# Kernel optimization log

Hardware: AMD Instinct MI355X
Metric: run time of the kernel (lower is better)

Reference implementation:

```python
import jax, jax.numpy as jnp
import numpy as np

# dims chosen per input_specs / init_kwargs
B, S, D_IN, UNITS, WIN = 4, 2048, 512, 64, 32
W = 2 * WIN + 1  # max window length


def setup_inputs() -> dict:
    key = jax.random.key(0)
    ks = jax.random.split(key, 8)
    p = lambda k, shape: jax.random.normal(k, shape, dtype=jnp.float32) * 0.02
    return {
        "query": jax.random.normal(ks[0], (B, S, D_IN), dtype=jnp.float32),
        "value": jax.random.normal(ks[1], (B, S, D_IN), dtype=jnp.float32),
        "Wq": p(ks[2], (D_IN, UNITS)), "bq": jnp.zeros((UNITS,), jnp.float32),
        "Wk": p(ks[3], (D_IN, UNITS)), "bk": jnp.zeros((UNITS,), jnp.float32),
        "Wv": p(ks[4], (D_IN, UNITS)), "bv": jnp.zeros((UNITS,), jnp.float32),
    }


def reference(query, value, Wq, bq, Wk, bk, Wv, bv):
    # Dense projections (query stream -> Q, value stream -> K and V)
    Q = query @ Wq + bq
    K = value @ Wk + bk
    V = value @ Wv + bv

    i = np.arange(S)
    start = np.maximum(i - WIN, 0)            # [S]
    end = np.minimum(i + WIN + 1, S)          # [S]
    lengths = end - start                      # [S] window length per position
    offsets = np.concatenate([[0], np.cumsum(lengths)[:-1]])
    L = int(lengths.sum())                     # total output seq length (concat of all windows)

    idx = start[:, None] + np.arange(W)[None, :]   # [S, W] window token indices
    valid = idx < end[:, None]                      # [S, W] which slots exist
    idx_c = np.minimum(idx, S - 1)                  # clamp for safe gather

    idx_c = jnp.asarray(idx_c)
    valid_j = jnp.asarray(valid)

    # Gather overlapping windows: [B, S, W, UNITS]
    Ql = Q[:, idx_c]
    Kl = K[:, idx_c]
    Vl = V[:, idx_c]

    # Faithful to original: ALL window rows act as queries for window i.
    scale = 1.0 / jnp.sqrt(jnp.asarray(UNITS, dtype=Q.dtype))
    scores = jnp.einsum("bswd,bsud->bswu", Ql, Kl) * scale  # [B, S, W, W]
    neg = jnp.finfo(scores.dtype).min
    scores = jnp.where(valid_j[None, :, None, :], scores, neg)  # mask padded keys
    weights = jax.nn.softmax(scores, axis=-1)
    out_local = jnp.einsum("bswu,bsud->bswd", weights, Vl)  # [B, S, W, UNITS]

    # Concat valid rows of every window along seq axis -> [B, L, UNITS]
    flat_pos = jnp.asarray(offsets)[:, None] + jnp.arange(W)[None, :]  # [S, W]
    flat_pos = jnp.where(valid_j, flat_pos, L)  # invalid rows dumped in slot L
    out = jnp.zeros((Q.shape[0], L + 1, UNITS), dtype=out_local.dtype)
    out = out.at[:, flat_pos.reshape(-1)].set(out_local.reshape(Q.shape[0], -1, UNITS))
    return out[:, :L]
```

## Files before the change

### kernel.cpp

```cpp
#include <hip/hip_runtime.h>
#include <hip/hip_bf16.h>

#define BB 4
#define SS 2048
#define DIN 512
#define UU 64
#define WINR 32
#define LTOT 132064
#define GQ 4
#define NWP 132

typedef __attribute__((ext_vector_type(8))) short short8;
typedef __attribute__((ext_vector_type(4))) float float4v;

static __device__ __forceinline__ ushort f2bf(float f) {
    union { __hip_bfloat16 h; ushort u; } c;
    c.h = __float2bfloat16(f);
    return c.u;
}
static __device__ __forceinline__ float bf2f(ushort u) {
    union { float f; uint v; } c;
    c.v = ((uint)u) << 16;
    return c.f;
}

__device__ __forceinline__ int offs_of(int s) {
    int a = s < (SS - 33) ? s : (SS - 33);
    int m = (s - 33) > 0 ? (s - 33) : 0;
    return a * (a - 1) / 2 + 33 * a + (s - a) * SS - m * (m + 1) / 2;
}

__global__ __launch_bounds__(256) void prep_w(
    const float* __restrict__ Wq, const float* __restrict__ Wk, const float* __restrict__ Wv,
    ushort* __restrict__ Wt)
{
    __shared__ float T[64][65];
    const int mtx = blockIdx.x >> 3;
    const int kc  = blockIdx.x & 7;
    const float* W = (mtx == 0) ? Wq : ((mtx == 1) ? Wk : Wv);
    const int tid = threadIdx.x;
    for (int idx = tid; idx < 64 * 64; idx += 256) {
        const int k = idx >> 6, n = idx & 63;
        T[n][k] = W[(size_t)(kc * 64 + k) * UU + n];
    }
    __syncthreads();
    for (int idx = tid; idx < 64 * 64; idx += 256) {
        const int n = idx >> 6, kl = idx & 63;
        Wt[(size_t)mtx * UU * DIN + (size_t)n * DIN + kc * 64 + kl] = f2bf(T[n][kl]);
    }
}

__global__ __launch_bounds__(64) void qkv_mfma(
    const float* __restrict__ query, const float* __restrict__ value,
    const ushort* __restrict__ Wt,
    const float* __restrict__ bq, const float* __restrict__ bk, const float* __restrict__ bv,
    float* __restrict__ Qs, ushort* __restrict__ Kf, ushort* __restrict__ Vf)
{
    const int bid = blockIdx.x;
    const int mtx = bid >> 9;
    const int rt  = bid & 511;
    const int lane = threadIdx.x;
    const int m16 = lane & 15, quad = lane >> 4;

    const float* X = (mtx == 0) ? query : value;
    const float* Xrow = X + (size_t)(rt * 16 + m16) * DIN + quad * 8;
    const ushort* Wm = Wt + (size_t)mtx * UU * DIN + (size_t)m16 * DIN + quad * 8;

    float4v acc[4];
#pragma unroll
    for (int nb = 0; nb < 4; ++nb) acc[nb] = (float4v){0.f, 0.f, 0.f, 0.f};

#pragma unroll
    for (int kk = 0; kk < 16; ++kk) {
        const float4 xa = *(const float4*)(Xrow + kk * 32);
        const float4 xb = *(const float4*)(Xrow + kk * 32 + 4);
        short8 a;
        a[0] = (short)f2bf(xa.x); a[1] = (short)f2bf(xa.y);
        a[2] = (short)f2bf(xa.z); a[3] = (short)f2bf(xa.w);
        a[4] = (short)f2bf(xb.x); a[5] = (short)f2bf(xb.y);
        a[6] = (short)f2bf(xb.z); a[7] = (short)f2bf(xb.w);
#pragma unroll
        for (int nb = 0; nb < 4; ++nb) {
            const short8 bfr = *(const short8*)(Wm + (size_t)nb * 16 * DIN + kk * 32);
            acc[nb] = __builtin_amdgcn_mfma_f32_16x16x32_bf16(a, bfr, acc[nb], 0, 0, 0);
        }
    }

    const float* bias = (mtx == 0) ? bq : ((mtx == 1) ? bk : bv);
    const int r0 = rt * 16 + quad * 4;
#pragma unroll
    for (int nb = 0; nb < 4; ++nb) {
        const int col = nb * 16 + m16;
        const float bv_ = bias[col];
        if (mtx == 0) {
#pragma unroll
            for (int reg = 0; reg < 4; ++reg)
                Qs[(size_t)(r0 + reg) * UU + col] = (acc[nb][reg] + bv_) * 0.125f;
        } else if (mtx == 1) {
#pragma unroll
            for (int reg = 0; reg < 4; ++reg)
                Kf[(size_t)(r0 + reg) * UU + col] = f2bf(acc[nb][reg] + bv_);
        } else {
#pragma unroll
            for (int reg = 0; reg < 4; ++reg)
                Vf[(size_t)(r0 + reg) * UU + col] = f2bf(acc[nb][reg] + bv_);
        }
    }
}

__global__ __launch_bounds__(512) void attn_kernel(
    const float* __restrict__ Qs, const ushort* __restrict__ Kf,
    const ushort* __restrict__ Vf, float* __restrict__ out)
{
    constexpr int STRIDE = 66;
    __shared__ ushort Kl[NWP * STRIDE];
    __shared__ ushort Vl[NWP * STRIDE];
    __shared__ float ev[GQ][NWP];
    __shared__ float qr[GQ][UU];

    const int blk = blockIdx.x;
    const int b = blk >> 9;
    const int q0 = (blk & 511) << 2;
    const int tid = threadIdx.x;

    const int j0 = max(q0 - 2 * WINR, 0);
    const int j1 = min(q0 + GQ - 1 + 2 * WINR + 1, SS);
    const int nw = j1 - j0;

    if (tid < GQ * UU) {
        const int g = tid >> 6, d = tid & 63;
        qr[g][d] = Qs[((size_t)b * SS + q0 + g) * UU + d];
    }
    const uint* Kg = (const uint*)(Kf + ((size_t)b * SS + j0) * UU);
    const uint* Vg = (const uint*)(Vf + ((size_t)b * SS + j0) * UU);
    for (int idx = tid; idx < nw * 32; idx += 512) {
        const int j = idx >> 5, d2 = idx & 31;
        ((uint*)(Kl + j * STRIDE))[d2] = Kg[idx];
        ((uint*)(Vl + j * STRIDE))[d2] = Vg[idx];
    }
    __syncthreads();

    for (int item = tid; item < GQ * NWP; item += 512) {
        const int g = item / NWP, jj = item - g * NWP;
        float e = 0.f;
        if (jj < nw) {
            const uint* kr = (const uint*)(Kl + jj * STRIDE);
            const float* q = qr[g];
            float dot = 0.f;
#pragma unroll
            for (int p = 0; p < UU / 2; ++p) {
                const uint kp = kr[p];
                dot = fmaf(q[2 * p],     bf2f((ushort)kp),         dot);
                dot = fmaf(q[2 * p + 1], bf2f((ushort)(kp >> 16)), dot);
            }
            e = __expf(dot);
        }
        ev[g][jj] = e;
    }
    __syncthreads();

    const int w = tid >> 6, lane = tid & 63;
    const int g = w >> 1, h = w & 1;
    const int qi = q0 + g;
    const int s_lo = max(qi - WINR, 0);
    const int s_hi = min(qi + WINR, SS - 1);
    const int ns = s_hi - s_lo + 1;
    const int half = (ns + 1) >> 1;
    const int sa = s_lo + h * half;
    const int sb = h ? s_hi : (s_lo + half - 1);

    int st = max(sa - WINR, 0);
    int en = min(sa + WINR + 1, SS);
    float acc = 0.f, den = 0.f;
    const float* evg = ev[g];
    for (int j = st; j < en; ++j) {
        const float e = evg[j - j0];
        acc = fmaf(e, bf2f(Vl[(j - j0) * STRIDE + lane]), acc);
        den += e;
    }
    int off = offs_of(sa);
    float* outb = out + (size_t)b * LTOT * UU;
    for (int s = sa;; ++s) {
        outb[(size_t)(off + (qi - st)) * UU + lane] = acc * __builtin_amdgcn_rcpf(den);
        if (s == sb) break;
        off += en - st;
        if (en < SS) {
            const float e = evg[en - j0];
            acc = fmaf(e, bf2f(Vl[(en - j0) * STRIDE + lane]), acc);
            den += e;
            ++en;
        }
        if (s + 1 > WINR) {
            const float e = evg[st - j0];
            acc = fmaf(-e, bf2f(Vl[(st - j0) * STRIDE + lane]), acc);
            den -= e;
            ++st;
        }
    }
}

extern "C" void kernel_launch(void* const* d_in, const int* in_sizes, int n_in,
                              void* d_out, int out_size, void* d_ws, size_t ws_size,
                              hipStream_t stream) {
    const float* query = (const float*)d_in[0];
    const float* value = (const float*)d_in[1];
    const float* Wq = (const float*)d_in[2];
    const float* bq = (const float*)d_in[3];
    const float* Wk = (const float*)d_in[4];
    const float* bk = (const float*)d_in[5];
    const float* Wv = (const float*)d_in[6];
    const float* bv = (const float*)d_in[7];
    float* out = (float*)d_out;

    float* Qs = (float*)d_ws;
    ushort* Kf = (ushort*)(Qs + (size_t)BB * SS * UU);
    ushort* Vf = Kf + (size_t)BB * SS * UU;
    ushort* Wt = (ushort*)((float*)d_out + (size_t)out_size) - (size_t)3 * UU * DIN;

    prep_w<<<24, 256, 0, stream>>>(Wq, Wk, Wv, Wt);
    qkv_mfma<<<3 * 512, 64, 0, stream>>>(query, value, Wt, bq, bk, bv, Qs, Kf, Vf);
    attn_kernel<<<BB * SS / GQ, 512, 0, stream>>>(Qs, Kf, Vf, out);
}
```

Measured before the change: 212.6 us.

## Split-K projection across four waves and process two query rows per attention wave

```diff
diff --git a/kernel.cpp b/kernel.cpp
--- a/kernel.cpp
+++ b/kernel.cpp
@@ -7,8 +7,9 @@
 #define UU 64
 #define WINR 32
 #define LTOT 132064
-#define GQ 4
-#define NWP 132
+#define GQ 16
+#define NWP 144
+#define KST 66
 
 typedef __attribute__((ext_vector_type(8))) short short8;
 typedef __attribute__((ext_vector_type(4))) float float4v;
@@ -50,28 +51,31 @@
     }
 }
 
-__global__ __launch_bounds__(64) void qkv_mfma(
+__global__ __launch_bounds__(256) void qkv_mfma(
     const float* __restrict__ query, const float* __restrict__ value,
     const ushort* __restrict__ Wt,
     const float* __restrict__ bq, const float* __restrict__ bk, const float* __restrict__ bv,
     float* __restrict__ Qs, ushort* __restrict__ Kf, ushort* __restrict__ Vf)
 {
+    __shared__ float red[4][16 * UU];
     const int bid = blockIdx.x;
     const int mtx = bid >> 9;
     const int rt  = bid & 511;
-    const int lane = threadIdx.x;
+    const int tid = threadIdx.x;
+    const int kq = tid >> 6;
+    const int lane = tid & 63;
     const int m16 = lane & 15, quad = lane >> 4;
 
     const float* X = (mtx == 0) ? query : value;
-    const float* Xrow = X + (size_t)(rt * 16 + m16) * DIN + quad * 8;
-    const ushort* Wm = Wt + (size_t)mtx * UU * DIN + (size_t)m16 * DIN + quad * 8;
+    const float* Xrow = X + (size_t)(rt * 16 + m16) * DIN + kq * 128 + quad * 8;
+    const ushort* Wm = Wt + (size_t)mtx * UU * DIN + (size_t)m16 * DIN + kq * 128 + quad * 8;
 
     float4v acc[4];
 #pragma unroll
     for (int nb = 0; nb < 4; ++nb) acc[nb] = (float4v){0.f, 0.f, 0.f, 0.f};
 
 #pragma unroll
-    for (int kk = 0; kk < 16; ++kk) {
+    for (int kk = 0; kk < 4; ++kk) {
         const float4 xa = *(const float4*)(Xrow + kk * 32);
         const float4 xb = *(const float4*)(Xrow + kk * 32 + 4);
         short8 a;
@@ -86,25 +90,23 @@
         }
     }
 
+#pragma unroll
+    for (int nb = 0; nb < 4; ++nb)
+#pragma unroll
+        for (int reg = 0; reg < 4; ++reg)
+            red[kq][(quad * 4 + reg) * UU + nb * 16 + m16] = acc[nb][reg];
+    __syncthreads();
+
     const float* bias = (mtx == 0) ? bq : ((mtx == 1) ? bk : bv);
-    const int r0 = rt * 16 + quad * 4;
-#pragma unroll
-    for (int nb = 0; nb < 4; ++nb) {
-        const int col = nb * 16 + m16;
-        const float bv_ = bias[col];
-        if (mtx == 0) {
-#pragma unroll
-            for (int reg = 0; reg < 4; ++reg)
-                Qs[(size_t)(r0 + reg) * UU + col] = (acc[nb][reg] + bv_) * 0.125f;
-        } else if (mtx == 1) {
-#pragma unroll
-            for (int reg = 0; reg < 4; ++reg)
-                Kf[(size_t)(r0 + reg) * UU + col] = f2bf(acc[nb][reg] + bv_);
-        } else {
-#pragma unroll
-            for (int reg = 0; reg < 4; ++reg)
-                Vf[(size_t)(r0 + reg) * UU + col] = f2bf(acc[nb][reg] + bv_);
-        }
+#pragma unroll
+    for (int i = 0; i < 4; ++i) {
+        const int e = tid + 256 * i;
+        const int col = e & 63, row = e >> 6;
+        float s = red[0][e] + red[1][e] + red[2][e] + red[3][e] + bias[col];
+        const size_t gi = (size_t)(rt * 16 + row) * UU + col;
+        if (mtx == 0)      Qs[gi] = s * 0.125f;
+        else if (mtx == 1) Kf[gi] = f2bf(s);
+        else               Vf[gi] = f2bf(s);
     }
 }
 
@@ -112,31 +114,29 @@
     const float* __restrict__ Qs, const ushort* __restrict__ Kf,
     const ushort* __restrict__ Vf, float* __restrict__ out)
 {
-    constexpr int STRIDE = 66;
-    __shared__ ushort Kl[NWP * STRIDE];
-    __shared__ ushort Vl[NWP * STRIDE];
-    __shared__ float ev[GQ][NWP];
-    __shared__ float qr[GQ][UU];
+    __shared__ ushort Kl[NWP * KST];
+    __shared__ ushort Vl[NWP * KST];
+    __shared__ float  ev[GQ][NWP];
+    __shared__ float  qr[GQ][UU];
 
     const int blk = blockIdx.x;
-    const int b = blk >> 9;
-    const int q0 = (blk & 511) << 2;
+    const int b = blk >> 7;
+    const int q0 = (blk & 127) << 4;
     const int tid = threadIdx.x;
 
     const int j0 = max(q0 - 2 * WINR, 0);
     const int j1 = min(q0 + GQ - 1 + 2 * WINR + 1, SS);
     const int nw = j1 - j0;
 
-    if (tid < GQ * UU) {
-        const int g = tid >> 6, d = tid & 63;
-        qr[g][d] = Qs[((size_t)b * SS + q0 + g) * UU + d];
-    }
+    for (int idx = tid; idx < GQ * UU; idx += 512)
+        qr[idx >> 6][idx & 63] = Qs[((size_t)b * SS + q0) * UU + idx];
+
     const uint* Kg = (const uint*)(Kf + ((size_t)b * SS + j0) * UU);
     const uint* Vg = (const uint*)(Vf + ((size_t)b * SS + j0) * UU);
     for (int idx = tid; idx < nw * 32; idx += 512) {
         const int j = idx >> 5, d2 = idx & 31;
-        ((uint*)(Kl + j * STRIDE))[d2] = Kg[idx];
-        ((uint*)(Vl + j * STRIDE))[d2] = Vg[idx];
+        ((uint*)(Kl + j * KST))[d2] = Kg[idx];
+        ((uint*)(Vl + j * KST))[d2] = Vg[idx];
     }
     __syncthreads();
 
@@ -144,7 +144,7 @@
         const int g = item / NWP, jj = item - g * NWP;
         float e = 0.f;
         if (jj < nw) {
-            const uint* kr = (const uint*)(Kl + jj * STRIDE);
+            const uint* kr = (const uint*)(Kl + jj * KST);
             const float* q = qr[g];
             float dot = 0.f;
 #pragma unroll
@@ -160,40 +160,42 @@
     __syncthreads();
 
     const int w = tid >> 6, lane = tid & 63;
-    const int g = w >> 1, h = w & 1;
-    const int qi = q0 + g;
-    const int s_lo = max(qi - WINR, 0);
-    const int s_hi = min(qi + WINR, SS - 1);
-    const int ns = s_hi - s_lo + 1;
-    const int half = (ns + 1) >> 1;
-    const int sa = s_lo + h * half;
-    const int sb = h ? s_hi : (s_lo + half - 1);
-
-    int st = max(sa - WINR, 0);
-    int en = min(sa + WINR + 1, SS);
-    float acc = 0.f, den = 0.f;
-    const float* evg = ev[g];
+    const int qA = q0 + 2 * w, qB = qA + 1;
+    const int sA = max(qA - WINR, 0);
+    const int sB = min(qB + WINR, SS - 1);
+    int st = max(sA - WINR, 0);
+    int en = min(sA + WINR + 1, SS);
+    const float* eA = ev[2 * w];
+    const float* eB = ev[2 * w + 1];
+
+    float accA = 0.f, denA = 0.f, accB = 0.f, denB = 0.f;
     for (int j = st; j < en; ++j) {
-        const float e = evg[j - j0];
-        acc = fmaf(e, bf2f(Vl[(j - j0) * STRIDE + lane]), acc);
-        den += e;
-    }
-    int off = offs_of(sa);
+        const float v = bf2f(Vl[(j - j0) * KST + lane]);
+        const float a = eA[j - j0], bw = eB[j - j0];
+        accA = fmaf(a, v, accA);  denA += a;
+        accB = fmaf(bw, v, accB); denB += bw;
+    }
+    int off = offs_of(sA);
     float* outb = out + (size_t)b * LTOT * UU;
-    for (int s = sa;; ++s) {
-        outb[(size_t)(off + (qi - st)) * UU + lane] = acc * __builtin_amdgcn_rcpf(den);
-        if (s == sb) break;
+    for (int s = sA;; ++s) {
+        if (s <= qA + WINR)
+            outb[(size_t)(off + qA - st) * UU + lane] = accA * __builtin_amdgcn_rcpf(denA);
+        if (s >= qB - WINR)
+            outb[(size_t)(off + qB - st) * UU + lane] = accB * __builtin_amdgcn_rcpf(denB);
+        if (s == sB) break;
         off += en - st;
         if (en < SS) {
-            const float e = evg[en - j0];
-            acc = fmaf(e, bf2f(Vl[(en - j0) * STRIDE + lane]), acc);
-            den += e;
+            const float v = bf2f(Vl[(en - j0) * KST + lane]);
+            const float a = eA[en - j0], bw = eB[en - j0];
+            accA = fmaf(a, v, accA);  denA += a;
+            accB = fmaf(bw, v, accB); denB += bw;
             ++en;
         }
         if (s + 1 > WINR) {
-            const float e = evg[st - j0];
-            acc = fmaf(-e, bf2f(Vl[(st - j0) * STRIDE + lane]), acc);
-            den -= e;
+            const float v = bf2f(Vl[(st - j0) * KST + lane]);
+            const float a = eA[st - j0], bw = eB[st - j0];
+            accA = fmaf(-a, v, accA);  denA -= a;
+            accB = fmaf(-bw, v, accB); denB -= bw;
             ++st;
         }
     }
@@ -218,6 +220,6 @@
     ushort* Wt = (ushort*)((float*)d_out + (size_t)out_size) - (size_t)3 * UU * DIN;
 
     prep_w<<<24, 256, 0, stream>>>(Wq, Wk, Wv, Wt);
-    qkv_mfma<<<3 * 512, 64, 0, stream>>>(query, value, Wt, bq, bk, bv, Qs, Kf, Vf);
+    qkv_mfma<<<3 * 512, 256, 0, stream>>>(query, value, Wt, bq, bk, bv, Qs, Kf, Vf);
     attn_kernel<<<BB * SS / GQ, 512, 0, stream>>>(Qs, Kf, Vf, out);
 }
```

Measured after the change: 213.0 us. No clear change (+0.2%).
